# Kernel tuning notes

Measured on AMD Instinct MI355X. Metric: run time of the kernel, lower is better.

## Reference

```python
import jax, jax.numpy as jnp
import numpy as np

MEL, EMB, PRE, RNN, ATT = 80, 256, 256, 1024, 128
LOC_FILTERS, LOC_KERNEL = 32, 31


def _dropout(x, p, key):
    keep = jax.random.bernoulli(key, 1.0 - p, x.shape)
    return jnp.where(keep, x / (1.0 - p), 0.0).astype(x.dtype)


def _lstm_cell(x, h, c, Wih, Whh, bih, bhh):
    # torch LSTMCell gate order: i, f, g, o
    gates = x @ Wih.T + h @ Whh.T + (bih + bhh)
    i, f, g, o = jnp.split(gates, 4, axis=-1)
    c_new = jax.nn.sigmoid(f) * c + jax.nn.sigmoid(i) * jnp.tanh(g)
    h_new = jax.nn.sigmoid(o) * jnp.tanh(c_new)
    return h_new, c_new


def setup_inputs() -> dict:
    key = jax.random.key(0)
    ks = jax.random.split(key, 24)
    r = lambda k, shape, fan: (jax.random.normal(k, shape, jnp.float32) / np.sqrt(fan))
    inp = {
        "embedding": jax.random.normal(ks[0], (32, 512, EMB), jnp.float32),
        "target_mels": jax.random.uniform(ks[1], (32, 400, MEL), jnp.float32),
        # PreNet
        "W1": r(ks[2], (PRE, MEL), MEL), "b1": jnp.zeros((PRE,), jnp.float32),
        "W2": r(ks[3], (PRE, PRE), PRE), "b2": jnp.zeros((PRE,), jnp.float32),
        # pre_rnn LSTMCell: input = pre_net_dim + embedding_dim = 512
        "Wih_pre": r(ks[4], (4 * RNN, PRE + EMB), PRE + EMB),
        "Whh_pre": r(ks[5], (4 * RNN, RNN), RNN),
        "bih_pre": jnp.zeros((4 * RNN,), jnp.float32),
        "bhh_pre": jnp.zeros((4 * RNN,), jnp.float32),
        # location-sensitive attention
        "Wq": r(ks[6], (ATT, RNN), RNN),
        "Wmem": r(ks[7], (ATT, EMB), EMB),
        "conv_w": r(ks[8], (LOC_FILTERS, 2, LOC_KERNEL), 2 * LOC_KERNEL),
        "Wloc": r(ks[9], (ATT, LOC_FILTERS), LOC_FILTERS),
        "v": r(ks[10], (ATT,), ATT),
        # post_rnn LSTMCell: input = rnn_dim + embedding_dim = 1280
        "Wih_post": r(ks[11], (4 * RNN, RNN + EMB), RNN + EMB),
        "Whh_post": r(ks[12], (4 * RNN, RNN), RNN),
        "bih_post": jnp.zeros((4 * RNN,), jnp.float32),
        "bhh_post": jnp.zeros((4 * RNN,), jnp.float32),
        # projections
        "Wmel": r(ks[13], (MEL, RNN + EMB), RNN + EMB), "bmel": jnp.zeros((MEL,), jnp.float32),
        "Wstop": r(ks[14], (1, RNN + EMB), RNN + EMB), "bstop": jnp.zeros((1,), jnp.float32),
    }
    return inp


def _decoder_forward(embedding, target_mels, W1, b1, W2, b2,
                     Wih_pre, Whh_pre, bih_pre, bhh_pre,
                     Wq, Wmem, conv_w, Wloc, v,
                     Wih_post, Whh_post, bih_post, bhh_post,
                     Wmel, bmel, Wstop, bstop):
    B, S, _ = embedding.shape
    T = target_mels.shape[1]
    # precompute processed memory [B, S, ATT]
    mem_proj = jnp.einsum("bse,ae->bsa", embedding, Wmem)
    # teacher-forced previous frames: zeros GO frame then target_mels[:, :-1]
    prev = jnp.concatenate([jnp.zeros((B, 1, MEL), target_mels.dtype), target_mels[:, :-1]], axis=1)
    prev = jnp.transpose(prev, (1, 0, 2))  # [T, B, MEL]
    base_key = jax.random.key(42)

    def step(carry, xs):
        c_pre, h_pre, c_post, h_post, context, a_w, a_sum = carry
        mel_prev, t = xs
        k1, k2, k3, k4 = jax.random.split(jax.random.fold_in(base_key, t), 4)
        # PreNet (dropout always on, p=0.5)
        p = _dropout(jax.nn.relu(mel_prev @ W1.T + b1), 0.5, k1)
        p = _dropout(jax.nn.relu(p @ W2.T + b2), 0.5, k2)
        # pre_rnn -- note original swaps (c, h) state names; replicated faithfully
        x = jnp.concatenate([p, context], axis=-1)
        c_pre, h_pre = _lstm_cell(x, c_pre, h_pre, Wih_pre, Whh_pre, bih_pre, bhh_pre)
        c_pre = _dropout(c_pre, 0.1, k3)
        # location-sensitive attention; query = h_pre (as in source)
        align_cat = jnp.stack([a_sum, a_w], axis=1)  # [B, 2, S]
        loc = jax.lax.conv_general_dilated(
            align_cat, conv_w, window_strides=(1,),
            padding=[(LOC_KERNEL // 2, LOC_KERNEL // 2)],
            dimension_numbers=("NCH", "OIH", "NCH"))  # [B, 32, S]
        q = h_pre @ Wq.T  # [B, ATT]
        loc_proj = jnp.einsum("bcs,ac->bsa", loc, Wloc)
        energies = jnp.einsum("bsa,a->bs", jnp.tanh(q[:, None, :] + mem_proj + loc_proj), v)
        a_w = jax.nn.softmax(energies, axis=-1)  # [B, S]
        context = jnp.einsum("bs,bse->be", a_w, embedding)
        a_sum = a_sum + a_w
        # post_rnn (same swapped-state convention)
        x2 = jnp.concatenate([h_pre, context], axis=-1)
        c_post, h_post = _lstm_cell(x2, c_post, h_post, Wih_post, Whh_post, bih_post, bhh_post)
        c_post = _dropout(c_post, 0.1, k4)
        out = jnp.concatenate([h_post, context], axis=-1)
        mel = jax.nn.sigmoid(out @ Wmel.T + bmel)
        stop = jax.nn.sigmoid(out @ Wstop.T + bstop)
        return (c_pre, h_pre, c_post, h_post, context, a_w, a_sum), (mel, stop)

    z = lambda d: jnp.zeros((B, d), embedding.dtype)
    carry0 = (z(RNN), z(RNN), z(RNN), z(RNN), z(EMB),
              jnp.zeros((B, S), embedding.dtype), jnp.zeros((B, S), embedding.dtype))
    _, (mels, stops) = jax.lax.scan(step, carry0, (prev, jnp.arange(T)))
    mel_frames = jnp.transpose(mels, (1, 0, 2))   # [B, T, MEL]
    stop_values = jnp.transpose(stops, (1, 0, 2))  # [B, T, 1]
    return mel_frames, stop_values


def reference(embedding, target_mels, W1, b1, W2, b2,
              Wih_pre, Whh_pre, bih_pre, bhh_pre,
              Wq, Wmem, conv_w, Wloc, v,
              Wih_post, Whh_post, bih_post, bhh_post,
              Wmel, bmel, Wstop, bstop):
    return _decoder_forward(embedding, target_mels, W1, b1, W2, b2,
                            Wih_pre, Whh_pre, bih_pre, bhh_pre,
                            Wq, Wmem, conv_w, Wloc, v,
                            Wih_post, Whh_post, bih_post, bhh_post,
                            Wmel, bmel, Wstop, bstop)
```

## Files before the change

kernel.cpp:

```cpp
#include <hip/hip_runtime.h>
#include <cstdint>
#include <cstddef>


#define BB   32
#define SS   512
#define EMBD 256
#define MELD 80
#define PRED 256
#define RNND 1024
#define ATTD 128
#define TT   400
#define NBLK 256

__device__ __forceinline__ void tf_block(uint32_t k0, uint32_t k1,
                                         uint32_t x0, uint32_t x1,
                                         uint32_t& o0, uint32_t& o1) {
  uint32_t ks2 = k0 ^ k1 ^ 0x1BD11BDAu;
  x0 += k0; x1 += k1;
#define TFR(r) { x0 += x1; x1 = (x1 << (r)) | (x1 >> (32 - (r))); x1 ^= x0; }
  TFR(13) TFR(15) TFR(26) TFR(6)
  x0 += k1;  x1 += ks2 + 1u;
  TFR(17) TFR(29) TFR(16) TFR(24)
  x0 += ks2; x1 += k0 + 2u;
  TFR(13) TFR(15) TFR(26) TFR(6)
  x0 += k0;  x1 += k1 + 3u;
  TFR(17) TFR(29) TFR(16) TFR(24)
  x0 += k1;  x1 += ks2 + 4u;
  TFR(13) TFR(15) TFR(26) TFR(6)
  x0 += ks2; x1 += k0 + 5u;
#undef TFR
  o0 = x0; o1 = x1;
}

__device__ __forceinline__ void subkey(int t, int j, uint32_t& k0, uint32_t& k1) {
  uint32_t a, b;
  tf_block(0u, 42u, 0u, (uint32_t)t, a, b);
  tf_block(a, b, 0u, (uint32_t)j, k0, k1);
}

__device__ __forceinline__ bool keep_draw(uint32_t k0, uint32_t k1,
                                          uint32_t idx, float pkeep) {
  uint32_t o0, o1;
  tf_block(k0, k1, 0u, idx, o0, o1);
  uint32_t bits = o0 ^ o1;
  float u = __uint_as_float((bits >> 9) | 0x3f800000u) - 1.0f;
  return u < pkeep;
}

__device__ __forceinline__ float sigm(float x) { return 1.0f / (1.0f + expf(-x)); }

__device__ __forceinline__ float llc_load1(const float* p) {
  float v;
  asm volatile("global_load_dword %0, %1, off sc0 sc1\ns_waitcnt vmcnt(0)"
               : "=v"(v) : "v"(p) : "memory");
  return v;
}
__device__ __forceinline__ void llc_load1x2(const float* p0, const float* p1,
                                            float& v0, float& v1) {
  asm volatile(
      "global_load_dword %0, %2, off sc0 sc1\n"
      "global_load_dword %1, %3, off sc0 sc1\n"
      "s_waitcnt vmcnt(0)"
      : "=&v"(v0), "=&v"(v1) : "v"(p0), "v"(p1) : "memory");
}
__device__ __forceinline__ float4 llc_load4(const float4* p) {
  float4 v;
  asm volatile("global_load_dwordx4 %0, %1, off sc0 sc1\ns_waitcnt vmcnt(0)"
               : "=v"(v) : "v"(p) : "memory");
  return v;
}
__device__ __forceinline__ void llc_store1(float* p, float v) {
  asm volatile("global_store_dword %0, %1, off sc0 sc1" :: "v"(p), "v"(v) : "memory");
}
__device__ __forceinline__ uint32_t llc_loadu(const uint32_t* p) {
  uint32_t v;
  asm volatile("global_load_dword %0, %1, off sc0 sc1\ns_waitcnt vmcnt(0)"
               : "=v"(v) : "v"(p) : "memory");
  return v;
}
__device__ __forceinline__ void llc_storeu(uint32_t* p, uint32_t v) {
  asm volatile("global_store_dword %0, %1, off sc0 sc1" :: "v"(p), "v"(v) : "memory");
}
__device__ __forceinline__ void llc_issue_f4(const float4* p, float4& v) {
  asm volatile("global_load_dwordx4 %0, %1, off sc0 sc1"
               : "=v"(v) : "v"(p) : "memory");
}
__device__ __forceinline__ void waitv0() {
  asm volatile("s_waitcnt vmcnt(0)" ::: "memory");
}

__device__ __forceinline__ void gsync(uint32_t* flags, uint32_t* gen, uint32_t& lgen) {
  asm volatile("s_waitcnt vmcnt(0)" ::: "memory");
  __syncthreads();
  lgen += 1u;
  if (blockIdx.x == 0) {
    if (threadIdx.x > 0) {
      uint32_t g;
      do {
        g = llc_loadu(&flags[threadIdx.x]);
        if (g >= lgen) break;
        __builtin_amdgcn_s_sleep(1);
      } while (true);
    }
    __syncthreads();
    if (threadIdx.x == 0) llc_storeu(gen, lgen);
  } else {
    if (threadIdx.x == 0) {
      llc_storeu(&flags[blockIdx.x], lgen);
      uint32_t g;
      do {
        g = llc_loadu(gen);
        if (g >= lgen) break;
        __builtin_amdgcn_s_sleep(2);
      } while (true);
    }
  }
  __syncthreads();
}

__global__ void init_kernel(float* statebase, int nstate) {
  int i = blockIdx.x * blockDim.x + threadIdx.x;
  if (i < nstate) statebase[i] = 0.0f;
}

__global__ __launch_bounds__(256) void prenet_kernel(
    const float* __restrict__ tmels, const float* __restrict__ W1,
    const float* __restrict__ b1, const float* __restrict__ W2,
    const float* __restrict__ b2, float* __restrict__ P_all) {
  __shared__ float melsh[MELD];
  __shared__ float h1sh[PRED];
  int blk = blockIdx.x, tid = threadIdx.x;
  int t = blk >> 5, b = blk & 31;
  if (tid < MELD)
    melsh[tid] = (t == 0) ? 0.0f : tmels[((size_t)b * TT + (t - 1)) * MELD + tid];
  __syncthreads();
  uint32_t k10, k11, k20, k21;
  subkey(t, 0, k10, k11);
  subkey(t, 1, k20, k21);
  {
    const float* wr = W1 + (size_t)tid * MELD;
    float acc = b1[tid];
    for (int m = 0; m < MELD; ++m) acc += melsh[m] * wr[m];
    acc = fmaxf(acc, 0.0f);
    bool kp = keep_draw(k10, k11, (uint32_t)(b * PRED + tid), 0.5f);
    h1sh[tid] = kp ? (acc / 0.5f) : 0.0f;
  }
  __syncthreads();
  {
    const float* wr = W2 + (size_t)tid * PRED;
    float acc = b2[tid];
    for (int k = 0; k < PRED; ++k) acc += h1sh[k] * wr[k];
    acc = fmaxf(acc, 0.0f);
    bool kp = keep_draw(k20, k21, (uint32_t)(b * PRED + tid), 0.5f);
    P_all[((size_t)t * BB + b) * PRED + tid] = kp ? (acc / 0.5f) : 0.0f;
  }
}

__global__ __launch_bounds__(128) void memproj_kernel(
    const float* __restrict__ emb, const float* __restrict__ Wmem,
    float* __restrict__ mp) {
  __shared__ float esh[EMBD];
  int blk = blockIdx.x, tid = threadIdx.x;
  const float* er = emb + (size_t)blk * EMBD;
  esh[tid] = er[tid];
  esh[tid + 128] = er[tid + 128];
  __syncthreads();
  const float4* wr = (const float4*)(Wmem + (size_t)tid * EMBD);
  const float4* xr = (const float4*)esh;
  float acc = 0.0f;
  for (int k4 = 0; k4 < EMBD / 4; ++k4) {
    float4 w = wr[k4], x = xr[k4];
    acc += w.x * x.x + w.y * x.y + w.z * x.z + w.w * x.w;
  }
  mp[(size_t)blk * ATTD + tid] = acc;
}

struct DecParams {
  const float *emb, *tmels;
  const float *Wih_pre, *Whh_pre, *bih_pre, *bhh_pre;
  const float *Wq, *conv_w, *Wloc, *vvec;
  const float *Wih_post, *Whh_post, *bih_post, *bhh_post;
  const float *Wmel, *bmel, *Wstop, *bstop;
  float *out;
  float *memproj, *P_all;
  float *Apre0, *Apre1, *Bpre0, *Bpre1;
  float *Apost0, *Apost1, *Bpost0, *Bpost1;
  float *ctx0, *ctx1, *aw0, *aw1, *asum0, *asum1;
  float *energ;
  uint32_t *flags;
};

template<int NJ, int SL, int KIH>
__device__ __forceinline__ void load_weights(
    float4 (&w)[4][18], float (&bs)[4], int hb, int tid,
    const float* __restrict__ Wih, const float* __restrict__ Whh,
    const float* __restrict__ bih, const float* __restrict__ bhh) {
  const int r = tid >> 5, s = tid & 31;
#pragma unroll
  for (int g = 0; g < 4; ++g) {
    int gcol = g * RNND + hb + r;
    bs[g] = bih[gcol] + bhh[gcol];
#pragma unroll
    for (int j4 = 0; j4 < NJ; ++j4) {
      float4 v4;
      {
        int k = s * SL + j4 * 4 + 0;
        v4.x = (k < KIH) ? Wih[(size_t)gcol * KIH + k] : Whh[(size_t)gcol * RNND + (k - KIH)];
      }
      {
        int k = s * SL + j4 * 4 + 1;
        v4.y = (k < KIH) ? Wih[(size_t)gcol * KIH + k] : Whh[(size_t)gcol * RNND + (k - KIH)];
      }
      {
        int k = s * SL + j4 * 4 + 2;
        v4.z = (k < KIH) ? Wih[(size_t)gcol * KIH + k] : Whh[(size_t)gcol * RNND + (k - KIH)];
      }
      {
        int k = s * SL + j4 * 4 + 3;
        v4.w = (k < KIH) ? Wih[(size_t)gcol * KIH + k] : Whh[(size_t)gcol * RNND + (k - KIH)];
      }
      w[g][j4] = v4;
    }
  }
}

template<int NJ, int SLP, int NL, int F4B, int L0, int S0>
__device__ __forceinline__ void lstm_phaseA(
    int tid, int hb, int tdraw, int jdraw,
    const float4 (&w)[4][18], const float (&bs)[4], float& c_state,
    const float* __restrict__ src0, const float* __restrict__ ctxp,
    const float* __restrict__ srcR,
    float* Aw, float* Bw, float* xs, float* gates) {
  const int r = tid >> 5;
  const int s = tid & 31;
  float4 rg[9];

  auto issue = [&](int c) {
#pragma unroll
    for (int i = 0; i < NL; ++i) {
      int flat = i * 256 + tid;
      int bl = flat / F4B;
      int k4 = flat - bl * F4B;
      int k = k4 * 4;
      int bg = c * 4 + bl;
      const float* sp;
      if (k < L0)            sp = src0 + (size_t)bg * S0 + k;
      else if (k < L0 + 256) sp = ctxp + bg * 256 + (k - L0);
      else                   sp = srcR + (size_t)bg * 1024 + (k - L0 - 256);
      llc_issue_f4((const float4*)sp, rg[i]);
    }
  };

  issue(0);
  for (int c = 0; c < 8; ++c) {
    __syncthreads();
    waitv0();
    __builtin_amdgcn_sched_barrier(0);
#pragma unroll
    for (int i = 0; i < NL; ++i) {
      int flat = i * 256 + tid;
      int bl = flat / F4B;
      int k4 = flat - bl * F4B;
      int slice = k4 / NJ;
      int j4 = k4 - slice * NJ;
      *(float4*)(xs + (bl * 32 + slice) * SLP + j4 * 4) = rg[i];
    }
    __syncthreads();
    if (c < 7) issue(c + 1);
#pragma unroll
    for (int bl = 0; bl < 4; ++bl) {
      const float4* xb = (const float4*)(xs + (bl * 32 + s) * SLP);
      float a0 = 0.f, a1 = 0.f, a2 = 0.f, a3 = 0.f;
#pragma unroll
      for (int j4 = 0; j4 < NJ; ++j4) {
        float4 x4 = xb[j4];
        a0 += w[0][j4].x * x4.x + w[0][j4].y * x4.y + w[0][j4].z * x4.z + w[0][j4].w * x4.w;
        a1 += w[1][j4].x * x4.x + w[1][j4].y * x4.y + w[1][j4].z * x4.z + w[1][j4].w * x4.w;
        a2 += w[2][j4].x * x4.x + w[2][j4].y * x4.y + w[2][j4].z * x4.z + w[2][j4].w * x4.w;
        a3 += w[3][j4].x * x4.x + w[3][j4].y * x4.y + w[3][j4].z * x4.z + w[3][j4].w * x4.w;
      }
#pragma unroll
      for (int m = 1; m < 32; m <<= 1) {
        a0 += __shfl_xor(a0, m);
        a1 += __shfl_xor(a1, m);
        a2 += __shfl_xor(a2, m);
        a3 += __shfl_xor(a3, m);
      }
      if (s == 0) {
        float4 g4;
        g4.x = a0 + bs[0]; g4.y = a1 + bs[1]; g4.z = a2 + bs[2]; g4.w = a3 + bs[3];
        ((float4*)gates)[(c * 4 + bl) * 8 + r] = g4;
      }
    }
  }
  __syncthreads();
  {
    const int hloc = r, bb = s;
    float4 g4 = ((const float4*)gates)[bb * 8 + hloc];
    uint32_t kk0, kk1;
    subkey(tdraw, jdraw, kk0, kk1);
    float iv = sigm(g4.x), fv = sigm(g4.y), gv = tanhf(g4.z), ov = sigm(g4.w);
    float c_new = fv * c_state + iv * gv;
    c_state = c_new;
    float h_new = ov * tanhf(c_new);
    bool kp = keep_draw(kk0, kk1, (uint32_t)(bb * RNND + hb + hloc), 0.9f);
    llc_store1(Aw + (size_t)bb * RNND + hb + hloc, kp ? (h_new / 0.9f) : 0.0f);
    llc_store1(Bw + (size_t)bb * RNND + hb + hloc, c_new);
  }
}

__global__ __launch_bounds__(256, 1) void decoder_persistent(DecParams p) {
  __shared__ __align__(16) float smem[10752];
  const int blk = blockIdx.x;
  const int tid = threadIdx.x;
  uint32_t* flags = p.flags;
  uint32_t* gen = p.flags + NBLK;
  uint32_t lgen = 0u;

  const bool is1 = (blk < 128);
  const int hb = (is1 ? blk : blk - 128) * 8;

  float4 w[4][18];
  float bs[4];
  if (is1) load_weights<12, 48, 512>(w, bs, hb, tid, p.Wih_pre, p.Whh_pre,
                                     p.bih_pre, p.bhh_pre);
  else     load_weights<18, 72, 1280>(w, bs, hb, tid, p.Wih_post, p.Whh_post,
                                      p.bih_post, p.bhh_post);
  float c_state = 0.0f;

  for (int t = 0; t <= TT; ++t) {
    const int rr = t & 1;
    const float* Apre_r  = rr ? p.Apre1  : p.Apre0;
    const float* Bpre_r  = rr ? p.Bpre1  : p.Bpre0;
    float*       Apre_w  = rr ? p.Apre0  : p.Apre1;
    float*       Bpre_w  = rr ? p.Bpre0  : p.Bpre1;
    const float* Apost_r = rr ? p.Apost0 : p.Apost1;
    float*       Apost_w = rr ? p.Apost1 : p.Apost0;
    float*       Bpost_w = rr ? p.Bpost1 : p.Bpost0;
    const float* ctx_r   = rr ? p.ctx1   : p.ctx0;
    float*       ctx_w   = rr ? p.ctx0   : p.ctx1;
    const float* aw_r    = rr ? p.aw1    : p.aw0;
    float*       aw_w    = rr ? p.aw0    : p.aw1;
    const float* asum_r  = rr ? p.asum1  : p.asum0;
    float*       asum_w  = rr ? p.asum0  : p.asum1;

    if (is1) {
      if (t < TT)
        lstm_phaseA<12, 52, 6, 384, 256, 256>(
            tid, hb, t, 2, w, bs, c_state,
            p.P_all + (size_t)t * BB * PRED, ctx_r, Apre_r,
            Apre_w, Bpre_w, smem, smem + 9728);
    } else {
      if (t > 0)
        lstm_phaseA<18, 76, 9, 576, 1024, 1024>(
            tid, hb, t - 1, 3, w, bs, c_state,
            Bpre_r, ctx_r, Apost_r,
            Apost_w, Bpost_w, smem, smem + 9728);
    }
    gsync(flags, gen, lgen);

    if (t < TT) {
      float* qsh   = smem;
      float* vsh   = smem + 128;
      float* awin  = smem + 256;
      float* aswin = smem + 352;
      float* wlocs = smem + 448;
      float* convs = smem + 4672;
      float* locs  = smem + 6656;
      float* hsh   = smem + 8960;
      float* qpart = smem + 9984;
      int b = blk >> 3, st = blk & 7, s0 = st * 64;
      {
        float4 hv = llc_load4(((const float4*)(Bpre_w + (size_t)b * RNND)) + tid);
        ((float4*)hsh)[tid] = hv;
      }
      if (tid < ATTD) vsh[tid] = p.vvec[tid];
      if (tid < 94) {
        int sg = s0 - 15 + tid;
        bool ok = (sg >= 0) && (sg < SS);
        float av = 0.0f, sv = 0.0f;
        if (ok) llc_load1x2(&aw_r[b * SS + sg], &asum_r[b * SS + sg], av, sv);
        awin[tid]  = av;
        aswin[tid] = sv;
      }
      for (int idx = tid; idx < ATTD * 32; idx += 256) {
        int a = idx >> 5, c = idx & 31;
        wlocs[a * 33 + c] = p.Wloc[a * 32 + c];
      }
      for (int idx = tid; idx < 32 * 62; idx += 256) convs[idx] = p.conv_w[idx];
      __syncthreads();
      {
        int a = tid & 127, half = tid >> 7;
        const float4* wr = ((const float4*)(p.Wq + (size_t)a * RNND)) + half * 128;
        const float4* xr = ((const float4*)hsh) + half * 128;
        float acc = 0.0f;
        for (int k4 = 0; k4 < 128; ++k4) {
          float4 wv = wr[k4], x = xr[k4];
          acc += wv.x * x.x + wv.y * x.y + wv.z * x.z + wv.w * x.w;
        }
        qpart[half * 128 + a] = acc;
      }
      __syncthreads();
      if (tid < 128) qsh[tid] = qpart[tid] + qpart[128 + tid];
      for (int idx = tid; idx < 64 * 32; idx += 256) {
        int sl = idx & 63, c = idx >> 6;
        const float* cw0 = &convs[c * 62];
        const float* cw1 = &convs[c * 62 + 31];
        float acc = 0.0f;
        for (int k = 0; k < 31; ++k)
          acc += cw0[k] * aswin[sl + k] + cw1[k] * awin[sl + k];
        locs[sl * 33 + c] = acc;
      }
      __syncthreads();
      int sl = tid >> 2, aq = tid & 3, sg = s0 + sl;
      const float* mp = p.memproj + ((size_t)b * SS + sg) * ATTD;
      float acc = 0.0f;
      const float* ls = &locs[sl * 33];
      for (int j = 0; j < 32; ++j) {
        int a = j * 4 + aq;
        const float* wl = &wlocs[a * 33];
        float lp = 0.0f;
#pragma unroll 8
        for (int c = 0; c < 32; ++c) lp += ls[c] * wl[c];
        acc += vsh[a] * tanhf(qsh[a] + mp[a] + lp);
      }
      acc += __shfl_down(acc, 2);
      acc += __shfl_down(acc, 1);
      if (aq == 0) llc_store1(&p.energ[b * SS + sg], acc);
    }
    gsync(flags, gen, lgen);

    if (t < TT && blk < 128) {
      float* psh   = smem;
      float* red   = smem + 512;
      float (*cpart)[64] = (float (*)[64])(smem + 768);
      int b = blk >> 2, ec = blk & 3;
      float e1, e2;
      llc_load1x2(&p.energ[b * SS + tid], &p.energ[b * SS + 256 + tid], e1, e2);
      red[tid] = fmaxf(e1, e2);
      __syncthreads();
      for (int s2 = 128; s2 > 0; s2 >>= 1) {
        if (tid < s2) red[tid] = fmaxf(red[tid], red[tid + s2]);
        __syncthreads();
      }
      float mx = red[0];
      __syncthreads();
      float p1 = expf(e1 - mx), p2 = expf(e2 - mx);
      psh[tid] = p1; psh[tid + 256] = p2;
      red[tid] = p1 + p2;
      __syncthreads();
      for (int s2 = 128; s2 > 0; s2 >>= 1) {
        if (tid < s2) red[tid] += red[tid + s2];
        __syncthreads();
      }
      float inv = 1.0f / red[0];
      int el = tid & 63, sq = tid >> 6;
      int e = ec * 64 + el;
      float acc = 0.0f;
      const float* ebase = p.emb + ((size_t)b * SS) * EMBD + e;
      for (int s2 = sq * 128; s2 < sq * 128 + 128; ++s2)
        acc += psh[s2] * ebase[(size_t)s2 * EMBD];
      cpart[sq][el] = acc;
      __syncthreads();
      if (tid < 64)
        llc_store1(&ctx_w[b * EMBD + ec * 64 + tid],
                   (cpart[0][tid] + cpart[1][tid] + cpart[2][tid] + cpart[3][tid]) * inv);
      if (ec == 0) {
        float a1 = p1 * inv, a2 = p2 * inv;
        float s1, s2v;
        llc_load1x2(&asum_r[b * SS + tid], &asum_r[b * SS + 256 + tid], s1, s2v);
        llc_store1(&aw_w[b * SS + tid], a1);
        llc_store1(&aw_w[b * SS + 256 + tid], a2);
        llc_store1(&asum_w[b * SS + tid], s1 + a1);
        llc_store1(&asum_w[b * SS + 256 + tid], s2v + a2);
      }
    } else if (t > 0 && blk >= 128 && blk < 160) {
      float* xall = smem;
      int b = blk - 128;
      int t_prev = t - 1;
      {
        float4 hv = llc_load4(((const float4*)(Bpost_w + (size_t)b * RNND)) + tid);
        ((float4*)xall)[tid] = hv;
        if (tid < 64) {
          float4 cv = llc_load4(((const float4*)(ctx_r + (size_t)b * EMBD)) + tid);
          ((float4*)(xall + RNND))[tid] = cv;
        }
      }
      __syncthreads();
      int o = tid;
      if (o <= 80) {
        const float* wrow = (o < 80) ? (p.Wmel + (size_t)o * 1280) : p.Wstop;
        const float4* w4 = (const float4*)wrow;
        const float4* x4 = (const float4*)xall;
        float acc = 0.0f;
        for (int k4 = 0; k4 < 320; ++k4) {
          float4 wv = w4[k4], x = x4[k4];
          acc += wv.x * x.x + wv.y * x.y + wv.z * x.z + wv.w * x.w;
        }
        acc += (o < 80) ? p.bmel[o] : p.bstop[0];
        float val = sigm(acc);
        if (o < 80)
          p.out[(size_t)b * (TT * MELD) + (size_t)t_prev * MELD + o] = val;
        else
          p.out[(size_t)BB * TT * MELD + (size_t)b * TT + t_prev] = val;
      }
    }
    gsync(flags, gen, lgen);
  }
}

extern "C" void kernel_launch(void* const* d_in, const int* in_sizes, int n_in,
                              void* d_out, int out_size, void* d_ws, size_t ws_size,
                              hipStream_t stream) {
  DecParams hp;
  hp.emb      = (const float*)d_in[0];
  hp.tmels    = (const float*)d_in[1];
  const float* W1 = (const float*)d_in[2];
  const float* b1 = (const float*)d_in[3];
  const float* W2 = (const float*)d_in[4];
  const float* b2 = (const float*)d_in[5];
  hp.Wih_pre  = (const float*)d_in[6];
  hp.Whh_pre  = (const float*)d_in[7];
  hp.bih_pre  = (const float*)d_in[8];
  hp.bhh_pre  = (const float*)d_in[9];
  hp.Wq       = (const float*)d_in[10];
  const float* Wmem = (const float*)d_in[11];
  hp.conv_w   = (const float*)d_in[12];
  hp.Wloc     = (const float*)d_in[13];
  hp.vvec     = (const float*)d_in[14];
  hp.Wih_post = (const float*)d_in[15];
  hp.Whh_post = (const float*)d_in[16];
  hp.bih_post = (const float*)d_in[17];
  hp.bhh_post = (const float*)d_in[18];
  hp.Wmel     = (const float*)d_in[19];
  hp.bmel     = (const float*)d_in[20];
  hp.Wstop    = (const float*)d_in[21];
  hp.bstop    = (const float*)d_in[22];
  hp.out = (float*)d_out;

  float* w = (float*)d_ws;
  size_t off = 0;
  auto carve = [&](size_t n) {
    float* ptr = w + off;
    off += (n + 63) & ~((size_t)63);
    return ptr;
  };
  hp.memproj = carve((size_t)BB * SS * ATTD);
  hp.P_all   = carve((size_t)TT * BB * PRED);
  size_t state_begin = off;
  hp.Apre0  = carve(BB * RNND); hp.Apre1  = carve(BB * RNND);
  hp.Bpre0  = carve(BB * RNND); hp.Bpre1  = carve(BB * RNND);
  hp.Apost0 = carve(BB * RNND); hp.Apost1 = carve(BB * RNND);
  hp.Bpost0 = carve(BB * RNND); hp.Bpost1 = carve(BB * RNND);
  hp.ctx0   = carve(BB * EMBD); hp.ctx1   = carve(BB * EMBD);
  hp.aw0    = carve(BB * SS);   hp.aw1    = carve(BB * SS);
  hp.asum0  = carve(BB * SS);   hp.asum1  = carve(BB * SS);
  hp.energ  = carve(BB * SS);
  hp.flags  = (uint32_t*)carve(512);
  size_t state_end = off;
  int nstate = (int)(state_end - state_begin);

  init_kernel<<<(nstate + 255) / 256, 256, 0, stream>>>(w + state_begin, nstate);
  prenet_kernel<<<TT * BB, 256, 0, stream>>>(hp.tmels, W1, b1, W2, b2, hp.P_all);
  memproj_kernel<<<BB * SS, 128, 0, stream>>>(hp.emb, Wmem, hp.memproj);
  decoder_persistent<<<NBLK, 256, 0, stream>>>(hp);

  (void)in_sizes; (void)n_in; (void)out_size; (void)ws_size;
}
```

Baseline: 68.85 ms.

## Use write-once per-timestep state buffers so loads can skip cache-coherent sc0 sc1

Adds a mode where the recurrent state (ctx, pre/post hidden outputs) is written to a separate slot per timestep instead of ping-pong double buffers. Each address is written only once, so reads of it can use ordinary cached loads rather than the sc0 sc1 coherent loads. This mode is enabled only when the workspace is large enough, and the non-coherent loads rely on no stale cache line being held for those fresh addresses. The shared-memory row pitch is also padded from 52/76 to 53/77, likely to reduce LDS bank conflicts, with the gate buffer moved accordingly.

```diff
diff --git a/kernel.cpp b/kernel.cpp
--- a/kernel.cpp
+++ b/kernel.cpp
@@ -12,6 +12,8 @@
 #define ATTD 128
 #define TT   400
 #define NBLK 256
+#define CTXS (BB * EMBD)
+#define HS   (BB * RNND)
 
 __device__ __forceinline__ void tf_block(uint32_t k0, uint32_t k1,
                                          uint32_t x0, uint32_t x1,
@@ -50,12 +52,6 @@
 
 __device__ __forceinline__ float sigm(float x) { return 1.0f / (1.0f + expf(-x)); }
 
-__device__ __forceinline__ float llc_load1(const float* p) {
-  float v;
-  asm volatile("global_load_dword %0, %1, off sc0 sc1\ns_waitcnt vmcnt(0)"
-               : "=v"(v) : "v"(p) : "memory");
-  return v;
-}
 __device__ __forceinline__ void llc_load1x2(const float* p0, const float* p1,
                                             float& v0, float& v1) {
   asm volatile(
@@ -82,9 +78,14 @@
 __device__ __forceinline__ void llc_storeu(uint32_t* p, uint32_t v) {
   asm volatile("global_store_dword %0, %1, off sc0 sc1" :: "v"(p), "v"(v) : "memory");
 }
-__device__ __forceinline__ void llc_issue_f4(const float4* p, float4& v) {
-  asm volatile("global_load_dwordx4 %0, %1, off sc0 sc1"
-               : "=v"(v) : "v"(p) : "memory");
+template<bool SC>
+__device__ __forceinline__ void issue_f4(const float4* p, float4& v) {
+  if constexpr (SC)
+    asm volatile("global_load_dwordx4 %0, %1, off sc0 sc1"
+                 : "=v"(v) : "v"(p) : "memory");
+  else
+    asm volatile("global_load_dwordx4 %0, %1, off"
+                 : "=v"(v) : "v"(p) : "memory");
 }
 __device__ __forceinline__ void waitv0() {
   asm volatile("s_waitcnt vmcnt(0)" ::: "memory");
@@ -186,9 +187,13 @@
   float *memproj, *P_all;
   float *Apre0, *Apre1, *Bpre0, *Bpre1;
   float *Apost0, *Apost1, *Bpost0, *Bpost1;
-  float *ctx0, *ctx1, *aw0, *aw1, *asum0, *asum1;
+  float *ctx0, *ctx1;
+  float *aw0, *aw1, *asum0, *asum1;
   float *energ;
+  float *ctx_all, *Apre_all, *Bpre_all, *Apost_all;
+  float *ctx_init, *Apre_init, *Apost_init;
   uint32_t *flags;
+  int mode;
 };
 
 template<int NJ, int SL, int KIH>
@@ -204,28 +209,20 @@
 #pragma unroll
     for (int j4 = 0; j4 < NJ; ++j4) {
       float4 v4;
-      {
-        int k = s * SL + j4 * 4 + 0;
-        v4.x = (k < KIH) ? Wih[(size_t)gcol * KIH + k] : Whh[(size_t)gcol * RNND + (k - KIH)];
-      }
-      {
-        int k = s * SL + j4 * 4 + 1;
-        v4.y = (k < KIH) ? Wih[(size_t)gcol * KIH + k] : Whh[(size_t)gcol * RNND + (k - KIH)];
-      }
-      {
-        int k = s * SL + j4 * 4 + 2;
-        v4.z = (k < KIH) ? Wih[(size_t)gcol * KIH + k] : Whh[(size_t)gcol * RNND + (k - KIH)];
-      }
-      {
-        int k = s * SL + j4 * 4 + 3;
-        v4.w = (k < KIH) ? Wih[(size_t)gcol * KIH + k] : Whh[(size_t)gcol * RNND + (k - KIH)];
-      }
+      { int k = s * SL + j4 * 4 + 0;
+        v4.x = (k < KIH) ? Wih[(size_t)gcol * KIH + k] : Whh[(size_t)gcol * RNND + (k - KIH)]; }
+      { int k = s * SL + j4 * 4 + 1;
+        v4.y = (k < KIH) ? Wih[(size_t)gcol * KIH + k] : Whh[(size_t)gcol * RNND + (k - KIH)]; }
+      { int k = s * SL + j4 * 4 + 2;
+        v4.z = (k < KIH) ? Wih[(size_t)gcol * KIH + k] : Whh[(size_t)gcol * RNND + (k - KIH)]; }
+      { int k = s * SL + j4 * 4 + 3;
+        v4.w = (k < KIH) ? Wih[(size_t)gcol * KIH + k] : Whh[(size_t)gcol * RNND + (k - KIH)]; }
       w[g][j4] = v4;
     }
   }
 }
 
-template<int NJ, int SLP, int NL, int F4B, int L0, int S0>
+template<bool SC, int NJ, int SLP, int NL, int F4B, int L0, int S0>
 __device__ __forceinline__ void lstm_phaseA(
     int tid, int hb, int tdraw, int jdraw,
     const float4 (&w)[4][18], const float (&bs)[4], float& c_state,
@@ -248,7 +245,7 @@
       if (k < L0)            sp = src0 + (size_t)bg * S0 + k;
       else if (k < L0 + 256) sp = ctxp + bg * 256 + (k - L0);
       else                   sp = srcR + (size_t)bg * 1024 + (k - L0 - 256);
-      llc_issue_f4((const float4*)sp, rg[i]);
+      issue_f4<SC>((const float4*)sp, rg[i]);
     }
   };
 
@@ -311,12 +308,13 @@
 }
 
 __global__ __launch_bounds__(256, 1) void decoder_persistent(DecParams p) {
-  __shared__ __align__(16) float smem[10752];
+  __shared__ __align__(16) float smem[11008];
   const int blk = blockIdx.x;
   const int tid = threadIdx.x;
   uint32_t* flags = p.flags;
   uint32_t* gen = p.flags + NBLK;
   uint32_t lgen = 0u;
+  const int mode = p.mode;
 
   const bool is1 = (blk < 128);
   const int hb = (is1 ? blk : blk - 128) * 8;
@@ -331,32 +329,68 @@
 
   for (int t = 0; t <= TT; ++t) {
     const int rr = t & 1;
-    const float* Apre_r  = rr ? p.Apre1  : p.Apre0;
-    const float* Bpre_r  = rr ? p.Bpre1  : p.Bpre0;
-    float*       Apre_w  = rr ? p.Apre0  : p.Apre1;
-    float*       Bpre_w  = rr ? p.Bpre0  : p.Bpre1;
-    const float* Apost_r = rr ? p.Apost0 : p.Apost1;
-    float*       Apost_w = rr ? p.Apost1 : p.Apost0;
-    float*       Bpost_w = rr ? p.Bpost1 : p.Bpost0;
-    const float* ctx_r   = rr ? p.ctx1   : p.ctx0;
-    float*       ctx_w   = rr ? p.ctx0   : p.ctx1;
-    const float* aw_r    = rr ? p.aw1    : p.aw0;
-    float*       aw_w    = rr ? p.aw0    : p.aw1;
-    const float* asum_r  = rr ? p.asum1  : p.asum0;
-    float*       asum_w  = rr ? p.asum0  : p.asum1;
+    const float *l1_ctx, *l1_srcR, *l2_src0, *l2_ctx, *l2_srcR;
+    float *l1_Aw, *l1_Bw, *l2_Aw, *l2_Bw;
+    const float *hq, *ctx_out;
+    float *ctxW, *bpostW;
+    const float* l1_src0 = p.P_all + (size_t)t * BB * PRED;
+    if (mode) {
+      l1_ctx  = t ? p.ctx_all  + (size_t)(t - 1) * CTXS : p.ctx_init;
+      l1_srcR = t ? p.Apre_all + (size_t)(t - 1) * HS   : p.Apre_init;
+      l1_Aw   = p.Apre_all + (size_t)t * HS;
+      l1_Bw   = p.Bpre_all + (size_t)t * HS;
+      int tau = t - 1;
+      l2_src0 = p.Bpre_all + (size_t)(tau < 0 ? 0 : tau) * HS;
+      l2_ctx  = (tau >= 0) ? p.ctx_all + (size_t)tau * CTXS : p.ctx_init;
+      l2_srcR = (tau >= 1) ? p.Apost_all + (size_t)(tau - 1) * HS : p.Apost_init;
+      l2_Aw   = p.Apost_all + (size_t)(tau < 0 ? 0 : tau) * HS;
+      l2_Bw   = p.Bpost0;
+      hq      = p.Bpre_all + (size_t)t * HS;
+      ctxW    = p.ctx_all + (size_t)t * CTXS;
+      ctx_out = t ? p.ctx_all + (size_t)(t - 1) * CTXS : p.ctx_init;
+      bpostW  = p.Bpost0;
+    } else {
+      l1_ctx  = rr ? p.ctx1 : p.ctx0;
+      l1_srcR = rr ? p.Apre1 : p.Apre0;
+      l1_Aw   = rr ? p.Apre0 : p.Apre1;
+      l1_Bw   = rr ? p.Bpre0 : p.Bpre1;
+      l2_src0 = rr ? p.Bpre1 : p.Bpre0;
+      l2_ctx  = rr ? p.ctx1 : p.ctx0;
+      l2_srcR = rr ? p.Apost0 : p.Apost1;
+      l2_Aw   = rr ? p.Apost1 : p.Apost0;
+      l2_Bw   = rr ? p.Bpost1 : p.Bpost0;
+      hq      = l1_Bw;
+      ctxW    = rr ? p.ctx0 : p.ctx1;
+      ctx_out = l2_ctx;
+      bpostW  = l2_Bw;
+    }
+    const float* aw_r   = rr ? p.aw1   : p.aw0;
+    float*       aw_w   = rr ? p.aw0   : p.aw1;
+    const float* asum_r = rr ? p.asum1 : p.asum0;
+    float*       asum_w = rr ? p.asum0 : p.asum1;
 
     if (is1) {
-      if (t < TT)
-        lstm_phaseA<12, 52, 6, 384, 256, 256>(
-            tid, hb, t, 2, w, bs, c_state,
-            p.P_all + (size_t)t * BB * PRED, ctx_r, Apre_r,
-            Apre_w, Bpre_w, smem, smem + 9728);
+      if (t < TT) {
+        if (mode)
+          lstm_phaseA<false, 12, 53, 6, 384, 256, 256>(
+              tid, hb, t, 2, w, bs, c_state, l1_src0, l1_ctx, l1_srcR,
+              l1_Aw, l1_Bw, smem, smem + 9920);
+        else
+          lstm_phaseA<true, 12, 53, 6, 384, 256, 256>(
+              tid, hb, t, 2, w, bs, c_state, l1_src0, l1_ctx, l1_srcR,
+              l1_Aw, l1_Bw, smem, smem + 9920);
+      }
     } else {
-      if (t > 0)
-        lstm_phaseA<18, 76, 9, 576, 1024, 1024>(
-            tid, hb, t - 1, 3, w, bs, c_state,
-            Bpre_r, ctx_r, Apost_r,
-            Apost_w, Bpost_w, smem, smem + 9728);
+      if (t > 0) {
+        if (mode)
+          lstm_phaseA<false, 18, 77, 9, 576, 1024, 1024>(
+              tid, hb, t - 1, 3, w, bs, c_state, l2_src0, l2_ctx, l2_srcR,
+              l2_Aw, l2_Bw, smem, smem + 9920);
+        else
+          lstm_phaseA<true, 18, 77, 9, 576, 1024, 1024>(
+              tid, hb, t - 1, 3, w, bs, c_state, l2_src0, l2_ctx, l2_srcR,
+              l2_Aw, l2_Bw, smem, smem + 9920);
+      }
     }
     gsync(flags, gen, lgen);
 
@@ -372,7 +406,9 @@
       float* qpart = smem + 9984;
       int b = blk >> 3, st = blk & 7, s0 = st * 64;
       {
-        float4 hv = llc_load4(((const float4*)(Bpre_w + (size_t)b * RNND)) + tid);
+        float4 hv;
+        if (mode) hv = ((const float4*)(hq + (size_t)b * RNND))[tid];
+        else      hv = llc_load4(((const float4*)(hq + (size_t)b * RNND)) + tid);
         ((float4*)hsh)[tid] = hv;
       }
       if (tid < ATTD) vsh[tid] = p.vvec[tid];
@@ -464,7 +500,7 @@
       cpart[sq][el] = acc;
       __syncthreads();
       if (tid < 64)
-        llc_store1(&ctx_w[b * EMBD + ec * 64 + tid],
+        llc_store1(&ctxW[b * EMBD + ec * 64 + tid],
                    (cpart[0][tid] + cpart[1][tid] + cpart[2][tid] + cpart[3][tid]) * inv);
       if (ec == 0) {
         float a1 = p1 * inv, a2 = p2 * inv;
@@ -480,10 +516,12 @@
       int b = blk - 128;
       int t_prev = t - 1;
       {
-        float4 hv = llc_load4(((const float4*)(Bpost_w + (size_t)b * RNND)) + tid);
+        float4 hv = llc_load4(((const float4*)(bpostW + (size_t)b * RNND)) + tid);
         ((float4*)xall)[tid] = hv;
         if (tid < 64) {
-          float4 cv = llc_load4(((const float4*)(ctx_r + (size_t)b * EMBD)) + tid);
+          float4 cv;
+          if (mode) cv = ((const float4*)(ctx_out + (size_t)b * EMBD))[tid];
+          else      cv = llc_load4(((const float4*)(ctx_out + (size_t)b * EMBD)) + tid);
           ((float4*)(xall + RNND))[tid] = cv;
         }
       }
@@ -549,22 +587,35 @@
   hp.memproj = carve((size_t)BB * SS * ATTD);
   hp.P_all   = carve((size_t)TT * BB * PRED);
   size_t state_begin = off;
-  hp.Apre0  = carve(BB * RNND); hp.Apre1  = carve(BB * RNND);
-  hp.Bpre0  = carve(BB * RNND); hp.Bpre1  = carve(BB * RNND);
-  hp.Apost0 = carve(BB * RNND); hp.Apost1 = carve(BB * RNND);
-  hp.Bpost0 = carve(BB * RNND); hp.Bpost1 = carve(BB * RNND);
-  hp.ctx0   = carve(BB * EMBD); hp.ctx1   = carve(BB * EMBD);
+  hp.Apre0  = carve(HS); hp.Apre1  = carve(HS);
+  hp.Bpre0  = carve(HS); hp.Bpre1  = carve(HS);
+  hp.Apost0 = carve(HS); hp.Apost1 = carve(HS);
+  hp.Bpost0 = carve(HS); hp.Bpost1 = carve(HS);
+  hp.ctx0   = carve(CTXS); hp.ctx1 = carve(CTXS);
   hp.aw0    = carve(BB * SS);   hp.aw1    = carve(BB * SS);
   hp.asum0  = carve(BB * SS);   hp.asum1  = carve(BB * SS);
+  hp.ctx_init  = carve(CTXS);
+  hp.Apre_init = carve(HS);
+  hp.Apost_init = carve(HS);
   hp.energ  = carve(BB * SS);
   hp.flags  = (uint32_t*)carve(512);
   size_t state_end = off;
   int nstate = (int)(state_end - state_begin);
+  hp.ctx_all   = carve((size_t)(TT + 1) * CTXS);
+  hp.Apre_all  = carve((size_t)(TT + 1) * HS);
+  hp.Bpre_all  = carve((size_t)(TT + 1) * HS);
+  hp.Apost_all = carve((size_t)(TT + 1) * HS);
+  size_t need_floats = off;
+  hp.mode = (ws_size / 4 >= need_floats) ? 1 : 0;
+  if (!hp.mode) {
+    hp.ctx_all = hp.ctx0; hp.Apre_all = hp.Apre0;
+    hp.Bpre_all = hp.Bpre0; hp.Apost_all = hp.Apost0;
+  }
 
   init_kernel<<<(nstate + 255) / 256, 256, 0, stream>>>(w + state_begin, nstate);
   prenet_kernel<<<TT * BB, 256, 0, stream>>>(hp.tmels, W1, b1, W2, b2, hp.P_all);
   memproj_kernel<<<BB * SS, 128, 0, stream>>>(hp.emb, Wmem, hp.memproj);
   decoder_persistent<<<NBLK, 256, 0, stream>>>(hp);
 
-  (void)in_sizes; (void)n_in; (void)out_size; (void)ws_size;
-}
+  (void)in_sizes; (void)n_in; (void)out_size;
+}
```

Result: slower. 84.84 ms (+23.2%).

## Stage recurrent state into per-XCD L2-resident buffers before LSTM phases

Applied to the files above, without the earlier changes.

Each block reads its XCD id from a hardware register and takes a rank within that XCD through an atomic counter. At every timestep the blocks of each XCD cooperatively copy the shared recurrent state (ctx, h_pre, c_pre, h_post) from coherent memory into a per-XCD buffer. The LSTM phases then read it with sc0-only loads that can hit the local L2, instead of many system-coherent sc0 sc1 loads going to the LLC. The cost is an extra grid-wide sync per step and a copy pass, and correctness now depends on how sc0 caching behaves within an XCD. Shared-memory row padding is also changed from 52/76 to 53/77.

```diff
diff --git a/kernel.cpp b/kernel.cpp
--- a/kernel.cpp
+++ b/kernel.cpp
@@ -12,6 +12,13 @@
 #define ATTD 128
 #define TT   400
 #define NBLK 256
+#define CTXS (BB * EMBD)
+#define HS   (BB * RNND)
+#define XB_FLOATS (CTXS + 3 * HS)
+#define XB_N4     (XB_FLOATS / 4)
+#define XB_STRIDE (XB_FLOATS + 64)
+
+typedef float nfloat4 __attribute__((ext_vector_type(4)));
 
 __device__ __forceinline__ void tf_block(uint32_t k0, uint32_t k1,
                                          uint32_t x0, uint32_t x1,
@@ -50,12 +57,6 @@
 
 __device__ __forceinline__ float sigm(float x) { return 1.0f / (1.0f + expf(-x)); }
 
-__device__ __forceinline__ float llc_load1(const float* p) {
-  float v;
-  asm volatile("global_load_dword %0, %1, off sc0 sc1\ns_waitcnt vmcnt(0)"
-               : "=v"(v) : "v"(p) : "memory");
-  return v;
-}
 __device__ __forceinline__ void llc_load1x2(const float* p0, const float* p1,
                                             float& v0, float& v1) {
   asm volatile(
@@ -82,8 +83,19 @@
 __device__ __forceinline__ void llc_storeu(uint32_t* p, uint32_t v) {
   asm volatile("global_store_dword %0, %1, off sc0 sc1" :: "v"(p), "v"(v) : "memory");
 }
-__device__ __forceinline__ void llc_issue_f4(const float4* p, float4& v) {
-  asm volatile("global_load_dwordx4 %0, %1, off sc0 sc1"
+__device__ __forceinline__ float4 sc0_load4(const float4* p) {
+  float4 v;
+  asm volatile("global_load_dwordx4 %0, %1, off sc0\ns_waitcnt vmcnt(0)"
+               : "=v"(v) : "v"(p) : "memory");
+  return v;
+}
+__device__ __forceinline__ void sc0_store4(float* p, float4 v) {
+  nfloat4 nv;
+  nv.x = v.x; nv.y = v.y; nv.z = v.z; nv.w = v.w;
+  asm volatile("global_store_dwordx4 %0, %1, off sc0" :: "v"(p), "v"(nv) : "memory");
+}
+__device__ __forceinline__ void issue_f4_sc0(const float4* p, float4& v) {
+  asm volatile("global_load_dwordx4 %0, %1, off sc0"
                : "=v"(v) : "v"(p) : "memory");
 }
 __device__ __forceinline__ void waitv0() {
@@ -188,7 +200,9 @@
   float *Apost0, *Apost1, *Bpost0, *Bpost1;
   float *ctx0, *ctx1, *aw0, *aw1, *asum0, *asum1;
   float *energ;
+  float *xcdbuf;
   uint32_t *flags;
+  uint32_t *xcdcnt;
 };
 
 template<int NJ, int SL, int KIH>
@@ -204,22 +218,14 @@
 #pragma unroll
     for (int j4 = 0; j4 < NJ; ++j4) {
       float4 v4;
-      {
-        int k = s * SL + j4 * 4 + 0;
-        v4.x = (k < KIH) ? Wih[(size_t)gcol * KIH + k] : Whh[(size_t)gcol * RNND + (k - KIH)];
-      }
-      {
-        int k = s * SL + j4 * 4 + 1;
-        v4.y = (k < KIH) ? Wih[(size_t)gcol * KIH + k] : Whh[(size_t)gcol * RNND + (k - KIH)];
-      }
-      {
-        int k = s * SL + j4 * 4 + 2;
-        v4.z = (k < KIH) ? Wih[(size_t)gcol * KIH + k] : Whh[(size_t)gcol * RNND + (k - KIH)];
-      }
-      {
-        int k = s * SL + j4 * 4 + 3;
-        v4.w = (k < KIH) ? Wih[(size_t)gcol * KIH + k] : Whh[(size_t)gcol * RNND + (k - KIH)];
-      }
+      { int k = s * SL + j4 * 4 + 0;
+        v4.x = (k < KIH) ? Wih[(size_t)gcol * KIH + k] : Whh[(size_t)gcol * RNND + (k - KIH)]; }
+      { int k = s * SL + j4 * 4 + 1;
+        v4.y = (k < KIH) ? Wih[(size_t)gcol * KIH + k] : Whh[(size_t)gcol * RNND + (k - KIH)]; }
+      { int k = s * SL + j4 * 4 + 2;
+        v4.z = (k < KIH) ? Wih[(size_t)gcol * KIH + k] : Whh[(size_t)gcol * RNND + (k - KIH)]; }
+      { int k = s * SL + j4 * 4 + 3;
+        v4.w = (k < KIH) ? Wih[(size_t)gcol * KIH + k] : Whh[(size_t)gcol * RNND + (k - KIH)]; }
       w[g][j4] = v4;
     }
   }
@@ -248,7 +254,7 @@
       if (k < L0)            sp = src0 + (size_t)bg * S0 + k;
       else if (k < L0 + 256) sp = ctxp + bg * 256 + (k - L0);
       else                   sp = srcR + (size_t)bg * 1024 + (k - L0 - 256);
-      llc_issue_f4((const float4*)sp, rg[i]);
+      issue_f4_sc0((const float4*)sp, rg[i]);
     }
   };
 
@@ -311,7 +317,8 @@
 }
 
 __global__ __launch_bounds__(256, 1) void decoder_persistent(DecParams p) {
-  __shared__ __align__(16) float smem[10752];
+  __shared__ __align__(16) float smem[11008];
+  __shared__ int sxcc, srank, snrank;
   const int blk = blockIdx.x;
   const int tid = threadIdx.x;
   uint32_t* flags = p.flags;
@@ -329,34 +336,67 @@
                                       p.bih_post, p.bhh_post);
   float c_state = 0.0f;
 
+  if (tid == 0) {
+    uint32_t x;
+    asm volatile("s_getreg_b32 %0, hwreg(20, 0, 32)" : "=s"(x));
+    x &= 7u;
+    sxcc = (int)x;
+    srank = (int)__hip_atomic_fetch_add(&p.xcdcnt[x], 1u, __ATOMIC_RELAXED,
+                                        __HIP_MEMORY_SCOPE_AGENT);
+  }
+  __syncthreads();
+  const int xcc = sxcc;
+  const int rank = srank;
+  gsync(flags, gen, lgen);
+  if (tid == 0) snrank = (int)llc_loadu(&p.xcdcnt[xcc]);
+  __syncthreads();
+  const int nrank = snrank;
+  float* xb = p.xcdbuf + (size_t)xcc * XB_STRIDE;
+  const float* xb_ctx   = xb;
+  const float* xb_apre  = xb + CTXS;
+  const float* xb_bpre  = xb + CTXS + HS;
+  const float* xb_apost = xb + CTXS + 2 * HS;
+
   for (int t = 0; t <= TT; ++t) {
     const int rr = t & 1;
-    const float* Apre_r  = rr ? p.Apre1  : p.Apre0;
-    const float* Bpre_r  = rr ? p.Bpre1  : p.Bpre0;
-    float*       Apre_w  = rr ? p.Apre0  : p.Apre1;
-    float*       Bpre_w  = rr ? p.Bpre0  : p.Bpre1;
-    const float* Apost_r = rr ? p.Apost0 : p.Apost1;
-    float*       Apost_w = rr ? p.Apost1 : p.Apost0;
-    float*       Bpost_w = rr ? p.Bpost1 : p.Bpost0;
-    const float* ctx_r   = rr ? p.ctx1   : p.ctx0;
-    float*       ctx_w   = rr ? p.ctx0   : p.ctx1;
-    const float* aw_r    = rr ? p.aw1    : p.aw0;
-    float*       aw_w    = rr ? p.aw0    : p.aw1;
-    const float* asum_r  = rr ? p.asum1  : p.asum0;
-    float*       asum_w  = rr ? p.asum0  : p.asum1;
+    const float* ctx_src   = rr ? p.ctx1  : p.ctx0;
+    const float* apre_src  = rr ? p.Apre1 : p.Apre0;
+    const float* bpre_src  = rr ? p.Bpre1 : p.Bpre0;
+    const float* apost_src = rr ? p.Apost0 : p.Apost1;
+    float* Apre_w  = rr ? p.Apre0  : p.Apre1;
+    float* Bpre_w  = rr ? p.Bpre0  : p.Bpre1;
+    float* Apost_w = rr ? p.Apost1 : p.Apost0;
+    float* Bpost_w = rr ? p.Bpost1 : p.Bpost0;
+    float* ctxW    = rr ? p.ctx0   : p.ctx1;
+    const float* aw_r   = rr ? p.aw1   : p.aw0;
+    float*       aw_w   = rr ? p.aw0   : p.aw1;
+    const float* asum_r = rr ? p.asum1 : p.asum0;
+    float*       asum_w = rr ? p.asum0 : p.asum1;
+
+    for (int i4 = rank * 256 + tid; i4 < XB_N4; i4 += nrank * 256) {
+      int k = i4 * 4;
+      const float* sp;
+      if (k < CTXS)               sp = ctx_src + k;
+      else if (k < CTXS + HS)     sp = apre_src + (k - CTXS);
+      else if (k < CTXS + 2 * HS) sp = bpre_src + (k - CTXS - HS);
+      else                        sp = apost_src + (k - CTXS - 2 * HS);
+      float4 v = llc_load4((const float4*)sp);
+      sc0_store4(xb + k, v);
+    }
+    gsync(flags, gen, lgen);
 
     if (is1) {
       if (t < TT)
-        lstm_phaseA<12, 52, 6, 384, 256, 256>(
+        lstm_phaseA<12, 53, 6, 384, 256, 256>(
             tid, hb, t, 2, w, bs, c_state,
-            p.P_all + (size_t)t * BB * PRED, ctx_r, Apre_r,
-            Apre_w, Bpre_w, smem, smem + 9728);
+            p.P_all + (size_t)t * BB * PRED, xb_ctx, xb_apre,
+            Apre_w, Bpre_w, smem, smem + 9920);
     } else {
       if (t > 0)
-        lstm_phaseA<18, 76, 9, 576, 1024, 1024>(
+        lstm_phaseA<18, 77, 9, 576, 1024, 1024>(
             tid, hb, t - 1, 3, w, bs, c_state,
-            Bpre_r, ctx_r, Apost_r,
-            Apost_w, Bpost_w, smem, smem + 9728);
+            xb_bpre, xb_ctx, xb_apost,
+            Apost_w, Bpost_w, smem, smem + 9920);
     }
     gsync(flags, gen, lgen);
 
@@ -464,7 +504,7 @@
       cpart[sq][el] = acc;
       __syncthreads();
       if (tid < 64)
-        llc_store1(&ctx_w[b * EMBD + ec * 64 + tid],
+        llc_store1(&ctxW[b * EMBD + ec * 64 + tid],
                    (cpart[0][tid] + cpart[1][tid] + cpart[2][tid] + cpart[3][tid]) * inv);
       if (ec == 0) {
         float a1 = p1 * inv, a2 = p2 * inv;
@@ -483,7 +523,7 @@
         float4 hv = llc_load4(((const float4*)(Bpost_w + (size_t)b * RNND)) + tid);
         ((float4*)xall)[tid] = hv;
         if (tid < 64) {
-          float4 cv = llc_load4(((const float4*)(ctx_r + (size_t)b * EMBD)) + tid);
+          float4 cv = sc0_load4(((const float4*)(xb_ctx + (size_t)b * EMBD)) + tid);
           ((float4*)(xall + RNND))[tid] = cv;
         }
       }
@@ -549,17 +589,19 @@
   hp.memproj = carve((size_t)BB * SS * ATTD);
   hp.P_all   = carve((size_t)TT * BB * PRED);
   size_t state_begin = off;
-  hp.Apre0  = carve(BB * RNND); hp.Apre1  = carve(BB * RNND);
-  hp.Bpre0  = carve(BB * RNND); hp.Bpre1  = carve(BB * RNND);
-  hp.Apost0 = carve(BB * RNND); hp.Apost1 = carve(BB * RNND);
-  hp.Bpost0 = carve(BB * RNND); hp.Bpost1 = carve(BB * RNND);
-  hp.ctx0   = carve(BB * EMBD); hp.ctx1   = carve(BB * EMBD);
+  hp.Apre0  = carve(HS); hp.Apre1  = carve(HS);
+  hp.Bpre0  = carve(HS); hp.Bpre1  = carve(HS);
+  hp.Apost0 = carve(HS); hp.Apost1 = carve(HS);
+  hp.Bpost0 = carve(HS); hp.Bpost1 = carve(HS);
+  hp.ctx0   = carve(CTXS); hp.ctx1 = carve(CTXS);
   hp.aw0    = carve(BB * SS);   hp.aw1    = carve(BB * SS);
   hp.asum0  = carve(BB * SS);   hp.asum1  = carve(BB * SS);
   hp.energ  = carve(BB * SS);
   hp.flags  = (uint32_t*)carve(512);
+  hp.xcdcnt = (uint32_t*)carve(64);
   size_t state_end = off;
   int nstate = (int)(state_end - state_begin);
+  hp.xcdbuf = carve((size_t)8 * XB_STRIDE);
 
   init_kernel<<<(nstate + 255) / 256, 256, 0, stream>>>(w + state_begin, nstate);
   prenet_kernel<<<TT * BB, 256, 0, stream>>>(hp.tmels, W1, b1, W2, b2, hp.P_all);
```

Result: slower. 85.09 ms (+23.6%).
